# Kernel tuning notes

Hardware: AMD Instinct MI355X
Metric: run time of the kernel (lower is better)

The kernel has to match this reference:

```python
import jax, jax.numpy as jnp
import numpy as np

N = 100000
E = 3200000
IN_C = 128
HID = 128
OUT_C = 1


def setup_inputs() -> dict:
    key = jax.random.key(0)
    ks = jax.random.split(key, 12)
    x = jax.random.normal(ks[0], (N, IN_C), dtype=jnp.float32)
    edge_index = jax.random.randint(ks[1], (2, E), 0, N, dtype=jnp.int64)
    # GCNConv weights (PyG: lin(x) then aggregate, plus bias)
    s1 = 1.0 / np.sqrt(IN_C)
    s2 = 1.0 / np.sqrt(HID)
    W1 = jax.random.uniform(ks[2], (IN_C, HID), jnp.float32, -s1, s1)
    b1 = jnp.zeros((HID,), jnp.float32)
    W2 = jax.random.uniform(ks[3], (HID, HID), jnp.float32, -s2, s2)
    b2 = jnp.zeros((HID,), jnp.float32)
    sl1 = 1.0 / np.sqrt(2 * HID + IN_C)
    Wl1 = jax.random.uniform(ks[4], (2 * HID + IN_C, HID), jnp.float32, -sl1, sl1)
    bl1 = jax.random.uniform(ks[5], (HID,), jnp.float32, -sl1, sl1)
    Wl2 = jax.random.uniform(ks[6], (HID, OUT_C), jnp.float32, -s2, s2)
    bl2 = jax.random.uniform(ks[7], (OUT_C,), jnp.float32, -s2, s2)
    return {"x": x, "edge_index": edge_index, "W1": W1, "b1": b1,
            "W2": W2, "b2": b2, "Wl1": Wl1, "bl1": bl1, "Wl2": Wl2, "bl2": bl2}


def _gcn_conv(x, W, b, row, col, deg_inv_sqrt):
    # GCNConv: D^{-1/2} (A + I) D^{-1/2} X W + b  (self-loops added with weight 1)
    xw = x @ W                                   # [N, H]
    norm = deg_inv_sqrt[row] * deg_inv_sqrt[col] # [E]
    msg = xw[row] * norm[:, None]                # gather + scale
    agg = jax.ops.segment_sum(msg, col, num_segments=x.shape[0])  # scatter-add
    agg = agg + xw * (deg_inv_sqrt * deg_inv_sqrt)[:, None]       # self-loop term
    return agg + b


def reference(x, edge_index, W1, b1, W2, b2, Wl1, bl1, Wl2, bl2):
    row, col = edge_index[0], edge_index[1]  # source -> target
    n = x.shape[0]
    # degree with self-loops (edge weight 1)
    deg = jax.ops.segment_sum(jnp.ones_like(col, dtype=x.dtype), col, num_segments=n) + 1.0
    deg_inv_sqrt = jax.lax.rsqrt(deg)
    x1 = jax.nn.relu(_gcn_conv(x, W1, b1, row, col, deg_inv_sqrt))
    # dropout is identity in eval mode
    x2 = jax.nn.relu(_gcn_conv(x1, W2, b2, row, col, deg_inv_sqrt))
    h = jnp.concatenate([x, x1, x2], axis=-1)   # [N, in + 2*hidden]
    h = jax.nn.relu(h @ Wl1 + bl1)
    out = jax.nn.sigmoid(h @ Wl2 + bl2)         # [N, 1]
    return out
```

## Files before the change

kernel.cpp:

```cpp
#include <hip/hip_runtime.h>
#include <hip/hip_fp16.h>
#include <math.h>


typedef __attribute__((ext_vector_type(8))) short bf16x8;
typedef __attribute__((ext_vector_type(4))) float f32x4;

#define BSHIFT 6
#define NB 256
#define MAXBUK 2048

__global__ __launch_bounds__(1024) void k_bhist(const int* __restrict__ col,
                                                int* __restrict__ partials,
                                                int nbuk, int e) {
    __shared__ int h[MAXBUK];
    int tid = threadIdx.x;
    for (int i = tid; i < nbuk; i += 1024) h[i] = 0;
    __syncthreads();
    for (long long i = (long long)blockIdx.x * 1024 + tid; i < e;
         i += (long long)NB * 1024)
        atomicAdd(&h[col[i] >> BSHIFT], 1);
    __syncthreads();
    for (int i = tid; i < nbuk; i += 1024)
        partials[(size_t)blockIdx.x * nbuk + i] = h[i];
}

__global__ __launch_bounds__(256) void k_bscan(int* __restrict__ partials,
                                               int* __restrict__ tot, int nbuk) {
    int gid = blockIdx.x * 256 + threadIdx.x;
    int w = gid >> 6, l = gid & 63;
    if (w >= nbuk) return;
    int carry = 0;
#pragma unroll
    for (int c = 0; c < NB / 64; ++c) {
        size_t idx = (size_t)(c * 64 + l) * nbuk + w;
        int v = partials[idx];
        int s = v;
        for (int d = 1; d < 64; d <<= 1) {
            int t = __shfl_up(s, d);
            if (l >= d) s += t;
        }
        partials[idx] = s - v + carry;
        carry += __shfl(s, 63);
    }
    if (l == 0) tot[w] = carry;
}

__global__ __launch_bounds__(256) void k_btot(const int* __restrict__ tot,
                                              int* __restrict__ base,
                                              int nbuk, int e) {
    __shared__ int s[256];
    __shared__ int carry_s;
    int t = threadIdx.x;
    if (t == 0) carry_s = 0;
    __syncthreads();
    for (int bb = 0; bb < nbuk; bb += 256) {
        int v = (bb + t < nbuk) ? tot[bb + t] : 0;
        s[t] = v;
        __syncthreads();
        for (int d = 1; d < 256; d <<= 1) {
            int a = (t >= d) ? s[t - d] : 0;
            __syncthreads();
            s[t] += a;
            __syncthreads();
        }
        int c0 = carry_s;
        if (bb + t < nbuk) base[bb + t] = s[t] - v + c0;
        __syncthreads();
        if (t == 0) carry_s = c0 + s[255];
        __syncthreads();
    }
    if (t == 0) base[nbuk] = e;
}

__global__ __launch_bounds__(1024) void k_bscatter(
    const int* __restrict__ row, const int* __restrict__ col,
    const int* __restrict__ base, const int* __restrict__ partials,
    int* __restrict__ bpack, int nbuk, int e) {
    __shared__ int cur[MAXBUK];
    int tid = threadIdx.x;
    for (int i = tid; i < nbuk; i += 1024)
        cur[i] = base[i] + partials[(size_t)blockIdx.x * nbuk + i];
    __syncthreads();
    for (long long i = (long long)blockIdx.x * 1024 + tid; i < e;
         i += (long long)NB * 1024) {
        int c = col[i];
        int pos = atomicAdd(&cur[c >> BSHIFT], 1);
        bpack[pos] = (row[i] << BSHIFT) | (c & 63);
    }
}

__global__ __launch_bounds__(256) void k_bfill(
    const int* __restrict__ bpack, const int* __restrict__ base,
    int* __restrict__ offs, int* __restrict__ srow,
    float* __restrict__ dinv, int n, int e, int nbuk) {
    __shared__ int h[64];
    __shared__ int cur[64];
    int b = blockIdx.x, tid = threadIdx.x;
    int nodeb = b << BSHIFT;
    if (tid < 64) h[tid] = 0;
    __syncthreads();
    int s0 = base[b], s1 = base[b + 1];
    for (int i = s0 + tid; i < s1; i += 256) atomicAdd(&h[bpack[i] & 63], 1);
    __syncthreads();
    if (tid < 64) {
        int v = h[tid];
        int s = v;
        for (int d = 1; d < 64; d <<= 1) {
            int t = __shfl_up(s, d);
            if (tid >= d) s += t;
        }
        int myoff = s0 + s - v;
        cur[tid] = myoff;
        int node = nodeb + tid;
        if (node < n) {
            offs[node] = myoff;
            dinv[node] = rsqrtf((float)v + 1.0f);
        }
    }
    if (b == nbuk - 1 && tid == 0) offs[n] = e;
    __syncthreads();
    for (int i = s0 + tid; i < s1; i += 256) {
        int p = bpack[i];
        int pos = atomicAdd(&cur[p & 63], 1);
        srow[pos] = p >> BSHIFT;
    }
}

__global__ void k_prep_w(const float* __restrict__ W1, const float* __restrict__ W2,
                         const float* __restrict__ Wl1, short* __restrict__ wb) {
    int i = blockIdx.x * blockDim.x + threadIdx.x;
    if (i >= 5 * 16384) return;
    int blk = i >> 14, rem = i & 16383;
    int k = rem >> 7, n = rem & 127;
    float v;
    if (blk == 0) v = W1[rem];
    else if (blk == 1) v = W2[rem];
    else v = Wl1[((blk - 2) * 128 + k) * 128 + n];
    unsigned u = __float_as_uint(v);
    unsigned hb = u & 0xFFFF0000u;
    float lo = v - __uint_as_float(hb);
    unsigned lb = __float_as_uint(lo);
    int kk = k >> 5, km = k & 31;
    int half = km >> 4, kq = km & 15, g = kq >> 2, j = kq & 3;
    int nt = n >> 4, c = n & 15;
    size_t idx = ((size_t)(kk * 8 + nt) * 64 + (g * 16 + c)) * 8 + (half * 4 + j);
    size_t base = (size_t)blk * 32768;
    wb[base + idx] = (short)(hb >> 16);
    wb[base + 16384 + idx] = (short)(lb >> 16);
}

__device__ inline short2 split_f(float x) {
    unsigned u = __float_as_uint(x);
    unsigned hb = u & 0xFFFF0000u;
    short h = (short)(u >> 16);
    short l = (short)(__float_as_uint(x - __uint_as_float(hb)) >> 16);
    return make_short2(h, l);
}

__device__ inline void loadA8(const void* src, int f16, size_t node, int off,
                              float* v) {
    if (f16) {
        const __half* p = (const __half*)src + node * 128 + off;
        int2 a = *(const int2*)p;
        int2 b = *(const int2*)(p + 16);
        const __half2* ah = (const __half2*)&a;
        const __half2* bh = (const __half2*)&b;
        float2 f;
        f = __half22float2(ah[0]); v[0] = f.x; v[1] = f.y;
        f = __half22float2(ah[1]); v[2] = f.x; v[3] = f.y;
        f = __half22float2(bh[0]); v[4] = f.x; v[5] = f.y;
        f = __half22float2(bh[1]); v[6] = f.x; v[7] = f.y;
    } else {
        const float* p = (const float*)src + node * 128 + off;
        float4 v0 = *(const float4*)p;
        float4 v1 = *(const float4*)(p + 16);
        v[0] = v0.x; v[1] = v0.y; v[2] = v0.z; v[3] = v0.w;
        v[4] = v1.x; v[5] = v1.y; v[6] = v1.z; v[7] = v1.w;
    }
}

__global__ __launch_bounds__(256) void k_gemm_mfma(
    const void* __restrict__ src0, const void* __restrict__ src1,
    const void* __restrict__ src2, const short* __restrict__ wb,
    const float* __restrict__ dscale, const float* __restrict__ bias,
    const float* __restrict__ wl2, const float* __restrict__ bl2,
    void* __restrict__ Y, int n, int nkb, int mode, int f16mask) {
    __shared__ short wl[32768];
    int tid = threadIdx.x;
    int wave = tid >> 6, lane = tid & 63;
    int g = lane >> 4, c = lane & 15;
    int base = blockIdx.x * 128 + wave * 32;

    f32x4 acc[2][8];
#pragma unroll
    for (int a = 0; a < 2; ++a)
#pragma unroll
        for (int b = 0; b < 8; ++b) acc[a][b] = (f32x4){0.f, 0.f, 0.f, 0.f};

    for (int kb = 0; kb < nkb; ++kb) {
        const void* src = (kb == 0) ? src0 : ((kb == 1) ? src1 : src2);
        int f16 = (f16mask >> kb) & 1;
        __syncthreads();
        {
            const int4* s = (const int4*)(wb + (size_t)kb * 32768);
            int4* d = (int4*)wl;
            for (int it = tid; it < 4096; it += 256) d[it] = s[it];
        }
        __syncthreads();
#pragma unroll
        for (int kk = 0; kk < 4; ++kk) {
            bf16x8 ah[2], al[2];
#pragma unroll
            for (int mf = 0; mf < 2; ++mf) {
                int node = base + mf * 16 + c;
                if (node >= n) node = n - 1;
                float v[8];
                loadA8(src, f16, (size_t)node, kk * 32 + g * 4, v);
                short2 s;
#pragma unroll
                for (int q = 0; q < 8; ++q) {
                    s = split_f(v[q]);
                    ah[mf][q] = s.x;
                    al[mf][q] = s.y;
                }
            }
#pragma unroll
            for (int nt = 0; nt < 8; ++nt) {
                int bidx = ((kk * 8 + nt) * 64 + lane) * 8;
                bf16x8 bh = *(const bf16x8*)&wl[bidx];
                bf16x8 bl = *(const bf16x8*)&wl[16384 + bidx];
#pragma unroll
                for (int mf = 0; mf < 2; ++mf) {
                    acc[mf][nt] = __builtin_amdgcn_mfma_f32_16x16x32_bf16(ah[mf], bh, acc[mf][nt], 0, 0, 0);
                    acc[mf][nt] = __builtin_amdgcn_mfma_f32_16x16x32_bf16(ah[mf], bl, acc[mf][nt], 0, 0, 0);
                    acc[mf][nt] = __builtin_amdgcn_mfma_f32_16x16x32_bf16(al[mf], bh, acc[mf][nt], 0, 0, 0);
                }
            }
        }
    }

    if (mode == 0) {
        __half* Yh = (__half*)Y;
#pragma unroll
        for (int mf = 0; mf < 2; ++mf) {
#pragma unroll
            for (int j = 0; j < 4; ++j) {
                int node = base + mf * 16 + g * 4 + j;
                if (node >= n) continue;
                float s = dscale[node];
#pragma unroll
                for (int nt = 0; nt < 8; ++nt)
                    Yh[(size_t)node * 128 + nt * 16 + c] =
                        __float2half(acc[mf][nt][j] * s);
            }
        }
    } else {
        float* Yf = (float*)Y;
        float wv[8], bv[8];
#pragma unroll
        for (int nt = 0; nt < 8; ++nt) {
            wv[nt] = wl2[nt * 16 + c];
            bv[nt] = bias[nt * 16 + c];
        }
        float blv = bl2[0];
#pragma unroll
        for (int mf = 0; mf < 2; ++mf) {
#pragma unroll
            for (int j = 0; j < 4; ++j) {
                float partial = 0.f;
#pragma unroll
                for (int nt = 0; nt < 8; ++nt)
                    partial += fmaxf(acc[mf][nt][j] + bv[nt], 0.f) * wv[nt];
#pragma unroll
                for (int m = 1; m < 16; m <<= 1) partial += __shfl_xor(partial, m);
                int node = base + mf * 16 + g * 4 + j;
                if (c == 0 && node < n)
                    Yf[node] = 1.f / (1.f + expf(-(partial + blv)));
            }
        }
    }
}

__global__ __launch_bounds__(256) void k_aggregate(
    const __half* __restrict__ xws, const float* __restrict__ dinv,
    const float* __restrict__ bias, const int* __restrict__ offs,
    const int* __restrict__ srow, __half* __restrict__ out, int n) {
    long long t = (long long)blockIdx.x * blockDim.x + threadIdx.x;
    int node = (int)(t >> 6);
    int l = (int)t & 63;
    if (node >= n) return;
    int start = offs[node], end = offs[node + 1];
    const __half* xb = xws + l * 2;
    float2 acc = __half22float2(*(const __half2*)(xb + (size_t)node * 128));
    int e = start;
    for (; e + 15 < end; e += 16) {
        int r[16];
#pragma unroll
        for (int q = 0; q < 16; ++q)
            r[q] = __builtin_nontemporal_load(&srow[e + q]);
        float2 v[16];
#pragma unroll
        for (int q = 0; q < 16; ++q)
            v[q] = __half22float2(*(const __half2*)(xb + (size_t)r[q] * 128));
        float sx = 0.f, sy = 0.f;
#pragma unroll
        for (int q = 0; q < 16; ++q) { sx += v[q].x; sy += v[q].y; }
        acc.x += sx;
        acc.y += sy;
    }
    for (; e + 7 < end; e += 8) {
        int r[8];
#pragma unroll
        for (int q = 0; q < 8; ++q)
            r[q] = __builtin_nontemporal_load(&srow[e + q]);
        float2 v[8];
#pragma unroll
        for (int q = 0; q < 8; ++q)
            v[q] = __half22float2(*(const __half2*)(xb + (size_t)r[q] * 128));
        float sx = 0.f, sy = 0.f;
#pragma unroll
        for (int q = 0; q < 8; ++q) { sx += v[q].x; sy += v[q].y; }
        acc.x += sx;
        acc.y += sy;
    }
    for (; e < end; ++e) {
        float2 v = __half22float2(*(const __half2*)(xb + (size_t)srow[e] * 128));
        acc.x += v.x;
        acc.y += v.y;
    }
    float s = dinv[node];
    float2 b = *(const float2*)(bias + l * 2);
    acc.x = fmaxf(fmaf(acc.x, s, b.x), 0.f);
    acc.y = fmaxf(fmaf(acc.y, s, b.y), 0.f);
    __half2 hv = __float22half2_rn(acc);
    unsigned u;
    __builtin_memcpy(&u, &hv, 4);
    __builtin_nontemporal_store(u, (unsigned*)(out + (size_t)node * 128 + l * 2));
}

extern "C" void kernel_launch(void* const* d_in, const int* in_sizes, int n_in,
                              void* d_out, int out_size, void* d_ws, size_t ws_size,
                              hipStream_t stream) {
    const float* x   = (const float*)d_in[0];
    const int*   ei  = (const int*)d_in[1];
    const float* W1  = (const float*)d_in[2];
    const float* b1  = (const float*)d_in[3];
    const float* W2  = (const float*)d_in[4];
    const float* b2  = (const float*)d_in[5];
    const float* Wl1 = (const float*)d_in[6];
    const float* bl1 = (const float*)d_in[7];
    const float* Wl2 = (const float*)d_in[8];
    const float* bl2 = (const float*)d_in[9];
    float* out = (float*)d_out;

    const int N = in_sizes[0] / 128;
    const int E = in_sizes[1] / 2;
    const int* row = ei;
    const int* col = ei + E;
    const int nbuk = (N + 63) >> 6;

    char* ws = (char*)d_ws;
    size_t off = 0;
    auto alloc = [&](size_t bytes) {
        void* p = ws + off;
        off += (bytes + 255) & ~(size_t)255;
        return p;
    };
    float*  dinv     = (float*)alloc((size_t)N * 4);
    int*    partials = (int*)alloc((size_t)NB * nbuk * 4);
    int*    tot      = (int*)alloc((size_t)nbuk * 4);
    int*    base     = (int*)alloc((size_t)(nbuk + 1) * 4);
    int*    offs     = (int*)alloc((size_t)(N + 1) * 4);
    int*    bpack    = (int*)alloc((size_t)E * 4);
    int*    srow     = (int*)alloc((size_t)E * 4);
    short*  wb       = (short*)alloc((size_t)5 * 32768 * 2);
    __half* bufA     = (__half*)alloc((size_t)N * 128 * 2);
    __half* bufB     = (__half*)alloc((size_t)N * 128 * 2);
    __half* bufC     = (__half*)alloc((size_t)N * 128 * 2);

    const int B = 256;
    int gG = (N + 127) / 128;
    int gP = (5 * 16384 + B - 1) / B;
    int gS = (nbuk * 64 + B - 1) / B;
    int gA = (int)(((long long)N * 64 + B - 1) / B);

    k_prep_w<<<gP, B, 0, stream>>>(W1, W2, Wl1, wb);
    k_bhist<<<NB, 1024, 0, stream>>>(col, partials, nbuk, E);
    k_bscan<<<gS, B, 0, stream>>>(partials, tot, nbuk);
    k_btot<<<1, B, 0, stream>>>(tot, base, nbuk, E);
    k_bscatter<<<NB, 1024, 0, stream>>>(row, col, base, partials, bpack, nbuk, E);
    k_bfill<<<nbuk, B, 0, stream>>>(bpack, base, offs, srow, dinv, N, E, nbuk);

    k_gemm_mfma<<<gG, B, 0, stream>>>(x, nullptr, nullptr, wb,
                                      dinv, nullptr, nullptr, nullptr,
                                      bufA, N, 1, 0, 0);
    k_aggregate<<<gA, B, 0, stream>>>(bufA, dinv, b1, offs, srow, bufB, N);

    k_gemm_mfma<<<gG, B, 0, stream>>>(bufB, nullptr, nullptr, wb + 32768,
                                      dinv, nullptr, nullptr, nullptr,
                                      bufA, N, 1, 0, 1);
    k_aggregate<<<gA, B, 0, stream>>>(bufA, dinv, b2, offs, srow, bufC, N);

    k_gemm_mfma<<<gG, B, 0, stream>>>(x, bufB, bufC, wb + 2 * 32768,
                                      nullptr, bl1, Wl2, bl2,
                                      out, N, 3, 1, 6);
}
```

Before: 431.6 us.

## Replace multi-pass bucket sort with fixed-capacity buckets and global atomics

```diff
diff --git a/kernel.cpp b/kernel.cpp
--- a/kernel.cpp
+++ b/kernel.cpp
@@ -7,101 +7,31 @@
 typedef __attribute__((ext_vector_type(4))) float f32x4;
 
 #define BSHIFT 6
-#define NB 256
-#define MAXBUK 2048
-
-__global__ __launch_bounds__(1024) void k_bhist(const int* __restrict__ col,
-                                                int* __restrict__ partials,
-                                                int nbuk, int e) {
-    __shared__ int h[MAXBUK];
-    int tid = threadIdx.x;
-    for (int i = tid; i < nbuk; i += 1024) h[i] = 0;
-    __syncthreads();
-    for (long long i = (long long)blockIdx.x * 1024 + tid; i < e;
-         i += (long long)NB * 1024)
-        atomicAdd(&h[col[i] >> BSHIFT], 1);
-    __syncthreads();
-    for (int i = tid; i < nbuk; i += 1024)
-        partials[(size_t)blockIdx.x * nbuk + i] = h[i];
-}
-
-__global__ __launch_bounds__(256) void k_bscan(int* __restrict__ partials,
-                                               int* __restrict__ tot, int nbuk) {
-    int gid = blockIdx.x * 256 + threadIdx.x;
-    int w = gid >> 6, l = gid & 63;
-    if (w >= nbuk) return;
-    int carry = 0;
-#pragma unroll
-    for (int c = 0; c < NB / 64; ++c) {
-        size_t idx = (size_t)(c * 64 + l) * nbuk + w;
-        int v = partials[idx];
-        int s = v;
-        for (int d = 1; d < 64; d <<= 1) {
-            int t = __shfl_up(s, d);
-            if (l >= d) s += t;
-        }
-        partials[idx] = s - v + carry;
-        carry += __shfl(s, 63);
-    }
-    if (l == 0) tot[w] = carry;
-}
-
-__global__ __launch_bounds__(256) void k_btot(const int* __restrict__ tot,
-                                              int* __restrict__ base,
-                                              int nbuk, int e) {
-    __shared__ int s[256];
-    __shared__ int carry_s;
-    int t = threadIdx.x;
-    if (t == 0) carry_s = 0;
-    __syncthreads();
-    for (int bb = 0; bb < nbuk; bb += 256) {
-        int v = (bb + t < nbuk) ? tot[bb + t] : 0;
-        s[t] = v;
-        __syncthreads();
-        for (int d = 1; d < 256; d <<= 1) {
-            int a = (t >= d) ? s[t - d] : 0;
-            __syncthreads();
-            s[t] += a;
-            __syncthreads();
-        }
-        int c0 = carry_s;
-        if (bb + t < nbuk) base[bb + t] = s[t] - v + c0;
-        __syncthreads();
-        if (t == 0) carry_s = c0 + s[255];
-        __syncthreads();
-    }
-    if (t == 0) base[nbuk] = e;
-}
-
-__global__ __launch_bounds__(1024) void k_bscatter(
-    const int* __restrict__ row, const int* __restrict__ col,
-    const int* __restrict__ base, const int* __restrict__ partials,
-    int* __restrict__ bpack, int nbuk, int e) {
-    __shared__ int cur[MAXBUK];
-    int tid = threadIdx.x;
-    for (int i = tid; i < nbuk; i += 1024)
-        cur[i] = base[i] + partials[(size_t)blockIdx.x * nbuk + i];
-    __syncthreads();
-    for (long long i = (long long)blockIdx.x * 1024 + tid; i < e;
-         i += (long long)NB * 1024) {
-        int c = col[i];
-        int pos = atomicAdd(&cur[c >> BSHIFT], 1);
-        bpack[pos] = (row[i] << BSHIFT) | (c & 63);
-    }
+#define CAP 4096
+
+__global__ void k_bscatter(const int* __restrict__ row, const int* __restrict__ col,
+                           int* __restrict__ qcur, int* __restrict__ bpack, int e) {
+    int i = blockIdx.x * blockDim.x + threadIdx.x;
+    if (i >= e) return;
+    int c = col[i];
+    int b = c >> BSHIFT;
+    int pos = atomicAdd(&qcur[b * 16], 1);
+    bpack[(size_t)b * CAP + pos] = (row[i] << BSHIFT) | (c & 63);
 }
 
 __global__ __launch_bounds__(256) void k_bfill(
-    const int* __restrict__ bpack, const int* __restrict__ base,
-    int* __restrict__ offs, int* __restrict__ srow,
-    float* __restrict__ dinv, int n, int e, int nbuk) {
+    const int* __restrict__ bpack, const int* __restrict__ qcur,
+    int2* __restrict__ offs2, int* __restrict__ srow,
+    float* __restrict__ dinv, int n) {
     __shared__ int h[64];
     __shared__ int cur[64];
     int b = blockIdx.x, tid = threadIdx.x;
     int nodeb = b << BSHIFT;
+    int cnt = qcur[b * 16];
+    int s0 = b * CAP;
     if (tid < 64) h[tid] = 0;
     __syncthreads();
-    int s0 = base[b], s1 = base[b + 1];
-    for (int i = s0 + tid; i < s1; i += 256) atomicAdd(&h[bpack[i] & 63], 1);
+    for (int i = tid; i < cnt; i += 256) atomicAdd(&h[bpack[s0 + i] & 63], 1);
     __syncthreads();
     if (tid < 64) {
         int v = h[tid];
@@ -110,18 +40,17 @@
             int t = __shfl_up(s, d);
             if (tid >= d) s += t;
         }
-        int myoff = s0 + s - v;
-        cur[tid] = myoff;
+        int local = s - v;
+        cur[tid] = s0 + local;
         int node = nodeb + tid;
         if (node < n) {
-            offs[node] = myoff;
+            offs2[node] = make_int2(s0 + local, s0 + local + v);
             dinv[node] = rsqrtf((float)v + 1.0f);
         }
     }
-    if (b == nbuk - 1 && tid == 0) offs[n] = e;
     __syncthreads();
-    for (int i = s0 + tid; i < s1; i += 256) {
-        int p = bpack[i];
+    for (int i = tid; i < cnt; i += 256) {
+        int p = bpack[s0 + i];
         int pos = atomicAdd(&cur[p & 63], 1);
         srow[pos] = p >> BSHIFT;
     }
@@ -284,13 +213,14 @@
 
 __global__ __launch_bounds__(256) void k_aggregate(
     const __half* __restrict__ xws, const float* __restrict__ dinv,
-    const float* __restrict__ bias, const int* __restrict__ offs,
+    const float* __restrict__ bias, const int2* __restrict__ offs2,
     const int* __restrict__ srow, __half* __restrict__ out, int n) {
     long long t = (long long)blockIdx.x * blockDim.x + threadIdx.x;
     int node = (int)(t >> 6);
     int l = (int)t & 63;
     if (node >= n) return;
-    int start = offs[node], end = offs[node + 1];
+    int2 se = offs2[node];
+    int start = se.x, end = se.y;
     const __half* xb = xws + l * 2;
     float2 acc = __half22float2(*(const __half2*)(xb + (size_t)node * 128));
     int e = start;
@@ -367,40 +297,36 @@
         off += (bytes + 255) & ~(size_t)255;
         return p;
     };
-    float*  dinv     = (float*)alloc((size_t)N * 4);
-    int*    partials = (int*)alloc((size_t)NB * nbuk * 4);
-    int*    tot      = (int*)alloc((size_t)nbuk * 4);
-    int*    base     = (int*)alloc((size_t)(nbuk + 1) * 4);
-    int*    offs     = (int*)alloc((size_t)(N + 1) * 4);
-    int*    bpack    = (int*)alloc((size_t)E * 4);
-    int*    srow     = (int*)alloc((size_t)E * 4);
-    short*  wb       = (short*)alloc((size_t)5 * 32768 * 2);
-    __half* bufA     = (__half*)alloc((size_t)N * 128 * 2);
-    __half* bufB     = (__half*)alloc((size_t)N * 128 * 2);
-    __half* bufC     = (__half*)alloc((size_t)N * 128 * 2);
+    float*  dinv  = (float*)alloc((size_t)N * 4);
+    int*    qcur  = (int*)alloc((size_t)nbuk * 16 * 4);
+    int2*   offs2 = (int2*)alloc((size_t)N * 8);
+    int*    bpack = (int*)alloc((size_t)nbuk * CAP * 4);
+    int*    srow  = (int*)alloc((size_t)nbuk * CAP * 4);
+    short*  wb    = (short*)alloc((size_t)5 * 32768 * 2);
+    __half* bufA  = (__half*)alloc((size_t)N * 128 * 2);
+    __half* bufB  = (__half*)alloc((size_t)N * 128 * 2);
+    __half* bufC  = (__half*)alloc((size_t)N * 128 * 2);
 
     const int B = 256;
     int gG = (N + 127) / 128;
     int gP = (5 * 16384 + B - 1) / B;
-    int gS = (nbuk * 64 + B - 1) / B;
+    int gE = (E + B - 1) / B;
     int gA = (int)(((long long)N * 64 + B - 1) / B);
 
+    hipMemsetAsync(qcur, 0, (size_t)nbuk * 16 * 4, stream);
     k_prep_w<<<gP, B, 0, stream>>>(W1, W2, Wl1, wb);
-    k_bhist<<<NB, 1024, 0, stream>>>(col, partials, nbuk, E);
-    k_bscan<<<gS, B, 0, stream>>>(partials, tot, nbuk);
-    k_btot<<<1, B, 0, stream>>>(tot, base, nbuk, E);
-    k_bscatter<<<NB, 1024, 0, stream>>>(row, col, base, partials, bpack, nbuk, E);
-    k_bfill<<<nbuk, B, 0, stream>>>(bpack, base, offs, srow, dinv, N, E, nbuk);
+    k_bscatter<<<gE, B, 0, stream>>>(row, col, qcur, bpack, E);
+    k_bfill<<<nbuk, B, 0, stream>>>(bpack, qcur, offs2, srow, dinv, N);
 
     k_gemm_mfma<<<gG, B, 0, stream>>>(x, nullptr, nullptr, wb,
                                       dinv, nullptr, nullptr, nullptr,
                                       bufA, N, 1, 0, 0);
-    k_aggregate<<<gA, B, 0, stream>>>(bufA, dinv, b1, offs, srow, bufB, N);
+    k_aggregate<<<gA, B, 0, stream>>>(bufA, dinv, b1, offs2, srow, bufB, N);
 
     k_gemm_mfma<<<gG, B, 0, stream>>>(bufB, nullptr, nullptr, wb + 32768,
                                       dinv, nullptr, nullptr, nullptr,
                                       bufA, N, 1, 0, 1);
-    k_aggregate<<<gA, B, 0, stream>>>(bufA, dinv, b2, offs, srow, bufC, N);
+    k_aggregate<<<gA, B, 0, stream>>>(bufA, dinv, b2, offs2, srow, bufC, N);
 
     k_gemm_mfma<<<gG, B, 0, stream>>>(x, bufB, bufC, wb + 2 * 32768,
                                       nullptr, bl1, Wl2, bl2,
```

New measurement: 580.1 us. +34.4%, slower.

## Split aggregation into two feature-half passes with edge-parallel half-waves

Applied to the files above, without the earlier changes.

```diff
diff --git a/kernel.cpp b/kernel.cpp
--- a/kernel.cpp
+++ b/kernel.cpp
@@ -285,35 +285,21 @@
 __global__ __launch_bounds__(256) void k_aggregate(
     const __half* __restrict__ xws, const float* __restrict__ dinv,
     const float* __restrict__ bias, const int* __restrict__ offs,
-    const int* __restrict__ srow, __half* __restrict__ out, int n) {
+    const int* __restrict__ srow, __half* __restrict__ out, int n, int coff) {
     long long t = (long long)blockIdx.x * blockDim.x + threadIdx.x;
     int node = (int)(t >> 6);
     int l = (int)t & 63;
     if (node >= n) return;
+    int sub = l >> 5, lc = l & 31;
     int start = offs[node], end = offs[node + 1];
-    const __half* xb = xws + l * 2;
-    float2 acc = __half22float2(*(const __half2*)(xb + (size_t)node * 128));
-    int e = start;
-    for (; e + 15 < end; e += 16) {
-        int r[16];
-#pragma unroll
-        for (int q = 0; q < 16; ++q)
-            r[q] = __builtin_nontemporal_load(&srow[e + q]);
-        float2 v[16];
-#pragma unroll
-        for (int q = 0; q < 16; ++q)
-            v[q] = __half22float2(*(const __half2*)(xb + (size_t)r[q] * 128));
-        float sx = 0.f, sy = 0.f;
-#pragma unroll
-        for (int q = 0; q < 16; ++q) { sx += v[q].x; sy += v[q].y; }
-        acc.x += sx;
-        acc.y += sy;
-    }
-    for (; e + 7 < end; e += 8) {
+    const __half* xb = xws + coff + lc * 2;
+    float2 acc = make_float2(0.f, 0.f);
+    int e = start + sub;
+    for (; e + 14 < end; e += 16) {
         int r[8];
 #pragma unroll
         for (int q = 0; q < 8; ++q)
-            r[q] = __builtin_nontemporal_load(&srow[e + q]);
+            r[q] = __builtin_nontemporal_load(&srow[e + 2 * q]);
         float2 v[8];
 #pragma unroll
         for (int q = 0; q < 8; ++q)
@@ -324,19 +310,26 @@
         acc.x += sx;
         acc.y += sy;
     }
-    for (; e < end; ++e) {
+    for (; e < end; e += 2) {
         float2 v = __half22float2(*(const __half2*)(xb + (size_t)srow[e] * 128));
         acc.x += v.x;
         acc.y += v.y;
     }
-    float s = dinv[node];
-    float2 b = *(const float2*)(bias + l * 2);
-    acc.x = fmaxf(fmaf(acc.x, s, b.x), 0.f);
-    acc.y = fmaxf(fmaf(acc.y, s, b.y), 0.f);
-    __half2 hv = __float22half2_rn(acc);
-    unsigned u;
-    __builtin_memcpy(&u, &hv, 4);
-    __builtin_nontemporal_store(u, (unsigned*)(out + (size_t)node * 128 + l * 2));
+    acc.x += __shfl_xor(acc.x, 32);
+    acc.y += __shfl_xor(acc.y, 32);
+    if (sub == 0) {
+        float2 self = __half22float2(*(const __half2*)(xb + (size_t)node * 128));
+        acc.x += self.x;
+        acc.y += self.y;
+        float s = dinv[node];
+        float2 b = *(const float2*)(bias + coff + lc * 2);
+        acc.x = fmaxf(fmaf(acc.x, s, b.x), 0.f);
+        acc.y = fmaxf(fmaf(acc.y, s, b.y), 0.f);
+        __half2 hv = __float22half2_rn(acc);
+        unsigned u;
+        __builtin_memcpy(&u, &hv, 4);
+        __builtin_nontemporal_store(u, (unsigned*)(out + (size_t)node * 128 + coff + lc * 2));
+    }
 }
 
 extern "C" void kernel_launch(void* const* d_in, const int* in_sizes, int n_in,
@@ -395,12 +388,14 @@
     k_gemm_mfma<<<gG, B, 0, stream>>>(x, nullptr, nullptr, wb,
                                       dinv, nullptr, nullptr, nullptr,
                                       bufA, N, 1, 0, 0);
-    k_aggregate<<<gA, B, 0, stream>>>(bufA, dinv, b1, offs, srow, bufB, N);
+    k_aggregate<<<gA, B, 0, stream>>>(bufA, dinv, b1, offs, srow, bufB, N, 0);
+    k_aggregate<<<gA, B, 0, stream>>>(bufA, dinv, b1, offs, srow, bufB, N, 64);
 
     k_gemm_mfma<<<gG, B, 0, stream>>>(bufB, nullptr, nullptr, wb + 32768,
                                       dinv, nullptr, nullptr, nullptr,
                                       bufA, N, 1, 0, 1);
-    k_aggregate<<<gA, B, 0, stream>>>(bufA, dinv, b2, offs, srow, bufC, N);
+    k_aggregate<<<gA, B, 0, stream>>>(bufA, dinv, b2, offs, srow, bufC, N, 0);
+    k_aggregate<<<gA, B, 0, stream>>>(bufA, dinv, b2, offs, srow, bufC, N, 64);
 
     k_gemm_mfma<<<gG, B, 0, stream>>>(x, bufB, bufC, wb + 2 * 32768,
                                       nullptr, bl1, Wl2, bl2,
```

After: 547.7 us. 26.9% more time.
